# Kernel tuning notes

Measured on AMD Instinct MI355X. Metric: run time of the kernel, lower is better.

The kernel has to match this reference:

```python
import jax, jax.numpy as jnp
import numpy as np

HIDDEN = 1024
INTER = 4096
N_EXPERTS = 8
TOP_K = 2
INIT_STD = 0.02


def setup_inputs() -> dict:
    key = jax.random.key(0)
    ks = jax.random.split(key, 6)
    x = jax.random.normal(ks[0], (2, 1024, HIDDEN), dtype=jnp.float32)
    Wg = jax.random.normal(ks[1], (N_EXPERTS, HIDDEN), dtype=jnp.float32) * INIT_STD
    # Expert MLP params, stacked over experts. W1: [E, H, I], W2: [E, I, H].
    W1 = jax.random.normal(ks[2], (N_EXPERTS, HIDDEN, INTER), dtype=jnp.float32) * INIT_STD
    b1 = jnp.zeros((N_EXPERTS, INTER), dtype=jnp.float32)
    W2 = jax.random.normal(ks[3], (N_EXPERTS, INTER, HIDDEN), dtype=jnp.float32) * INIT_STD
    b2 = jnp.zeros((N_EXPERTS, HIDDEN), dtype=jnp.float32)
    return {"x": x, "Wg": Wg, "W1": W1, "b1": b1, "W2": W2, "b2": b2}


def reference(x, Wg, W1, b1, W2, b2):
    orig_shape = x.shape
    xt = x.reshape(-1, HIDDEN)              # [T, H]
    T = xt.shape[0]

    # Gating: top-k logits -> softmax over the k selected experts.
    logits = xt @ Wg.T                      # [T, E]
    topk_logits, topk_idx = jax.lax.top_k(logits, TOP_K)   # [T, K]
    w = jax.nn.softmax(topk_logits, axis=-1)               # [T, K]

    # Scatter top-k weights into a dense [T, E] gate matrix (zeros elsewhere).
    rows = jnp.arange(T)[:, None]
    gates = jnp.zeros((T, N_EXPERTS), xt.dtype).at[rows, topk_idx].add(w)

    # Dense expert compute (mathematically identical: non-selected experts get
    # gate weight 0). Expert MLP: Linear -> GELU (exact, erf) -> Linear.
    h = jnp.einsum('th,ehi->tei', xt, W1) + b1             # [T, E, I]
    h = jax.nn.gelu(h, approximate=False)
    o = jnp.einsum('tei,eih->teh', h, W2) + b2             # [T, E, H]
    y = jnp.einsum('te,teh->th', gates, o)                 # [T, H]
    return y.reshape(orig_shape)
```

## Files before the change

kernel.cpp:

```cpp
#include <hip/hip_runtime.h>
#include <hip/hip_bf16.h>

#define HID 1024
#define INTER 4096
#define NE 8
#define NTOK 2048
#define MAXROWS 5120

typedef __attribute__((ext_vector_type(8))) short short8v;
typedef __attribute__((ext_vector_type(4))) short short4v;
typedef __attribute__((ext_vector_type(4))) float f32x4;

__device__ __forceinline__ unsigned short f2bf(float f) {
  unsigned int u = __builtin_bit_cast(unsigned int, f);
  u = (u + 0x7FFFu + ((u >> 16) & 1u)) >> 16;
  return (unsigned short)u;
}
__device__ __forceinline__ float bf2f(unsigned short s) {
  unsigned int u = ((unsigned int)s) << 16;
  return __builtin_bit_cast(float, u);
}

typedef const __attribute__((address_space(1))) unsigned int* gas_t;
typedef __attribute__((address_space(3))) unsigned int* las_t;
__device__ __forceinline__ void gld16(const unsigned short* g, unsigned short* l) {
  __builtin_amdgcn_global_load_lds((gas_t)(const void*)g, (las_t)(void*)l, 16, 0, 0);
}

__device__ __forceinline__ void tconv_tile(const float* __restrict__ in,
                                           unsigned short* __restrict__ out,
                                           int R, int C, int bx, int by, int z,
                                           float* __restrict__ t) {
  const int r0 = by * 64, c0 = bx * 64;
  const int tr = threadIdx.x / 16;
  const int tc = (threadIdx.x % 16) * 4;
  const float* ip = in + ((size_t)z * R + r0) * (size_t)C + c0;
#pragma unroll
  for (int p = 0; p < 4; ++p) {
    f32x4 v = *(const f32x4*)&ip[(size_t)(p * 16 + tr) * C + tc];
    t[(p * 16 + tr) * 65 + tc + 0] = v[0];
    t[(p * 16 + tr) * 65 + tc + 1] = v[1];
    t[(p * 16 + tr) * 65 + tc + 2] = v[2];
    t[(p * 16 + tr) * 65 + tc + 3] = v[3];
  }
  __syncthreads();
  unsigned short* op = out + ((size_t)z * C + c0) * (size_t)R + r0;
#pragma unroll
  for (int p = 0; p < 4; ++p) {
    int c = p * 16 + tr;
    unsigned int a0 = (unsigned int)f2bf(t[(tc + 0) * 65 + c]) |
                      ((unsigned int)f2bf(t[(tc + 1) * 65 + c]) << 16);
    unsigned int a1 = (unsigned int)f2bf(t[(tc + 2) * 65 + c]) |
                      ((unsigned int)f2bf(t[(tc + 3) * 65 + c]) << 16);
    uint2 val; val.x = a0; val.y = a1;
    *(uint2*)&op[(size_t)c * R + tc] = val;
  }
}

__global__ __launch_bounds__(256) void prep_kernel(const float* __restrict__ x,
                                                   const float* __restrict__ W1,
                                                   const float* __restrict__ wg,
                                                   unsigned short* __restrict__ xb,
                                                   unsigned short* __restrict__ w1t,
                                                   int* __restrict__ tok_e,
                                                   float* __restrict__ tok_w) {
  __shared__ float sh[64 * 65];
  int bid = blockIdx.x;
  if (bid < 2048) {
    size_t i = (size_t)bid * 256 + threadIdx.x;
    f32x4 v = *(const f32x4*)&x[i * 4];
    uint2 r;
    r.x = (unsigned int)f2bf(v[0]) | ((unsigned int)f2bf(v[1]) << 16);
    r.y = (unsigned int)f2bf(v[2]) | ((unsigned int)f2bf(v[3]) << 16);
    *(uint2*)&xb[i * 4] = r;
    return;
  }
  bid -= 2048;
  if (bid < 8192) {
    tconv_tile(W1, w1t, HID, INTER, bid % 64, (bid / 64) % 16, bid / 1024, sh);
    return;
  }
  bid -= 8192;
  {
    const int t = bid;
    float acc[NE];
#pragma unroll
    for (int e = 0; e < NE; ++e) acc[e] = 0.f;
    for (int k = threadIdx.x; k < HID; k += 256) {
      float xv = x[(size_t)t * HID + k];
#pragma unroll
      for (int e = 0; e < NE; ++e) acc[e] += xv * wg[e * HID + k];
    }
#pragma unroll
    for (int e = 0; e < NE; ++e) {
#pragma unroll
      for (int off = 32; off >= 1; off >>= 1) acc[e] += __shfl_xor(acc[e], off, 64);
    }
    float* red = sh;
    const int wave = threadIdx.x >> 6, lane = threadIdx.x & 63;
    if (lane == 0) {
#pragma unroll
      for (int e = 0; e < NE; ++e) red[wave * NE + e] = acc[e];
    }
    __syncthreads();
    if (threadIdx.x == 0) {
      float l[NE];
#pragma unroll
      for (int e = 0; e < NE; ++e)
        l[e] = red[0 * NE + e] + red[1 * NE + e] + red[2 * NE + e] + red[3 * NE + e];
      int i0 = 0;
#pragma unroll
      for (int e = 1; e < NE; ++e) if (l[e] > l[i0]) i0 = e;
      int i1 = -1;
#pragma unroll
      for (int e = 0; e < NE; ++e) {
        if (e == i0) continue;
        if (i1 < 0 || l[e] > l[i1]) i1 = e;
      }
      float e1 = __expf(l[i1] - l[i0]);
      float w0 = 1.f / (1.f + e1);
      tok_e[t * 2 + 0] = i0;
      tok_e[t * 2 + 1] = i1;
      tok_w[t * 2 + 0] = w0;
      tok_w[t * 2 + 1] = 1.f - w0;
    }
  }
}

__global__ __launch_bounds__(512) void routing_kernel(const int* __restrict__ tok_e,
                                                      int* __restrict__ list_tok,
                                                      int* __restrict__ tok_gslot,
                                                      int* __restrict__ offs_out) {
  __shared__ int cnts[NE];
  __shared__ int offs_s[NE + 1];
  const int e = threadIdx.x >> 6, lane = threadIdx.x & 63;
  int c = 0;
  for (int base = 0; base < NTOK; base += 64) {
    int tok = base + lane;
    int e0 = tok_e[tok * 2], e1 = tok_e[tok * 2 + 1];
    bool m = (e0 == e) || (e1 == e);
    unsigned long long mask = __ballot(m);
    c += __popcll(mask);
  }
  if (lane == 0) cnts[e] = c;
  __syncthreads();
  if (threadIdx.x == 0) {
    int o = 0;
    for (int i = 0; i < NE; ++i) { offs_s[i] = o; o += (cnts[i] + 127) & ~127; }
    offs_s[NE] = o;
    for (int i = 0; i <= NE; ++i) offs_out[i] = offs_s[i];
  }
  __syncthreads();
  const int off = offs_s[e];
  int run = 0;
  for (int base = 0; base < NTOK; base += 64) {
    int tok = base + lane;
    int e0 = tok_e[tok * 2], e1 = tok_e[tok * 2 + 1];
    bool m = (e0 == e) || (e1 == e);
    unsigned long long mask = __ballot(m);
    int pos = run + __popcll(mask & ((1ull << lane) - 1ull));
    if (m) {
      int gs = off + pos;
      list_tok[gs] = tok;
      tok_gslot[tok * 2 + ((e0 == e) ? 0 : 1)] = gs;
    }
    run += __popcll(mask);
  }
  const int cnt = cnts[e];
  const int padded = (cnt + 127) & ~127;
  for (int p = cnt + lane; p < padded; p += 64) list_tok[off + p] = 0;
}

template <int KTOT, int NTOT, bool FIRST, int NSPLIT, int TCONVN>
__global__ __launch_bounds__(256, 3) void moe_gemm(const unsigned short* __restrict__ Abase,
                                                   const unsigned short* __restrict__ Bbase,
                                                   const float* __restrict__ bias,
                                                   const int* __restrict__ list_tok,
                                                   const int* __restrict__ offs,
                                                   void* __restrict__ outp,
                                                   const float* __restrict__ W2f,
                                                   unsigned short* __restrict__ w2t) {
  constexpr int KS = KTOT / NSPLIT;
  constexpr int NT = KS / 32;
  constexpr int nM = MAXROWS / 128;
  constexpr int nN = NTOT / 128;
  constexpr int NWG_GEMM = nN * nM * NSPLIT;
  __shared__ __align__(16) unsigned short lds[3][2][4096];

  if (TCONVN != 0 && blockIdx.x >= NWG_GEMM) {
    int t = blockIdx.x - NWG_GEMM;
    tconv_tile(W2f, w2t, INTER, HID, t % 16, (t / 16) % 64, t / 1024,
               (float*)&lds[0][0][0]);
    return;
  }

  int wg = blockIdx.x;
  wg = (wg & 7) * (NWG_GEMM >> 3) + (wg >> 3);
  const int ks = (NSPLIT > 1) ? (wg / (nM * nN)) : 0;
  const int rem = wg % (nM * nN);
  const int mt = rem % nM;
  const int nt = rem / nM;
  const int grow0 = mt * 128;
  if (grow0 >= offs[NE]) return;
  int e = 0;
#pragma unroll
  for (int i = 1; i < NE; ++i) if (grow0 >= offs[i]) e = i;
  const int n0 = nt * 128;
  const int k0 = ks * KS;

  const int tid = threadIdx.x;
  const int wave = tid >> 6, lane = tid & 63;

  const int srow = tid >> 2;
  const int skc = (((tid & 3) ^ ((srow >> 1) & 3)) * 8);
  const unsigned short* ag[2];
  const unsigned short* bg[2];
#pragma unroll
  for (int j = 0; j < 2; ++j) {
    const int row = srow + j * 64;
    size_t arow;
    if (FIRST) arow = (size_t)list_tok[grow0 + row] * KTOT;
    else       arow = (size_t)(grow0 + row) * KTOT;
    ag[j] = Abase + arow + k0 + skc;
    bg[j] = Bbase + (size_t)e * NTOT * KTOT + (size_t)(n0 + row) * KTOT + k0 + skc;
  }
  const int wbase = wave * 512;

  const int wm = wave >> 1, wn = wave & 1;
  const int fr = lane & 15;
  const int q = lane >> 4;
  int aoff[4], boff[4];
#pragma unroll
  for (int m = 0; m < 4; ++m) {
    const int row = wm * 64 + m * 16 + fr;
    aoff[m] = row * 32 + ((q ^ ((row >> 1) & 3)) * 8);
  }
#pragma unroll
  for (int n = 0; n < 4; ++n) {
    const int row = wn * 64 + n * 16 + fr;
    boff[n] = row * 32 + ((q ^ ((row >> 1) & 3)) * 8);
  }

  f32x4 acc[4][4] = {};

#define STAGE(S, SLOT)                                             \
  {                                                                \
    gld16(ag[0] + (S) * 32, &lds[SLOT][0][wbase]);                 \
    gld16(ag[1] + (S) * 32, &lds[SLOT][0][wbase + 2048]);          \
    gld16(bg[0] + (S) * 32, &lds[SLOT][1][wbase]);                 \
    gld16(bg[1] + (S) * 32, &lds[SLOT][1][wbase + 2048]);          \
  }

#define KITER(S, SL, DO_STAGE, VMSTR)                                 \
  {                                                                   \
    asm volatile("s_waitcnt vmcnt(" VMSTR ")" ::: "memory");          \
    asm volatile("s_barrier" ::: "memory");                           \
    const unsigned short* A = &lds[SL][0][0];                         \
    const unsigned short* B = &lds[SL][1][0];                         \
    short8v af[4], bf[4];                                             \
    _Pragma("unroll")                                                 \
    for (int m = 0; m < 4; ++m) af[m] = *(const short8v*)&A[aoff[m]]; \
    _Pragma("unroll")                                                 \
    for (int n = 0; n < 4; ++n) bf[n] = *(const short8v*)&B[boff[n]]; \
    if (DO_STAGE) {                                                   \
      int s2 = (SL) + 2; if (s2 >= 3) s2 -= 3;                        \
      STAGE((S) + 2, s2);                                             \
    }                                                                 \
    __builtin_amdgcn_s_setprio(1);                                    \
    _Pragma("unroll")                                                 \
    for (int n = 0; n < 4; ++n)                                       \
      _Pragma("unroll")                                               \
      for (int m = 0; m < 4; ++m)                                     \
        acc[m][n] = __builtin_amdgcn_mfma_f32_16x16x32_bf16(af[m], bf[n], acc[m][n], 0, 0, 0); \
    __builtin_amdgcn_s_setprio(0);                                    \
  }

  STAGE(0, 0);
  STAGE(1, 1);

  int sl = 0;
  for (int s = 0; s < NT - 2; ++s) {
    KITER(s, sl, true, "4");
    sl = sl + 1; if (sl >= 3) sl = 0;
  }
  KITER(NT - 2, sl, false, "4");
  sl = sl + 1; if (sl >= 3) sl = 0;
  KITER(NT - 1, sl, false, "0");

#undef KITER
#undef STAGE

  const int r4 = lane >> 4;
#pragma unroll
  for (int m = 0; m < 4; ++m) {
#pragma unroll
    for (int n = 0; n < 4; ++n) {
      const int gcol = n0 + wn * 64 + n * 16 + fr;
      float bv = 0.f;
      if (FIRST) bv = bias[e * NTOT + gcol];
#pragma unroll
      for (int r = 0; r < 4; ++r) {
        const int grow = grow0 + wm * 64 + m * 16 + r4 * 4 + r;
        float v = acc[m][n][r] + bv;
        if (FIRST) {
          v = 0.5f * v * (1.0f + erff(v * 0.70710678118654752f));
          ((unsigned short*)outp)[(size_t)grow * NTOT + gcol] = f2bf(v);
        } else {
          ((unsigned short*)outp)[((size_t)ks * MAXROWS + grow) * NTOT + gcol] = f2bf(v);
        }
      }
    }
  }
}

template <int NSPLIT>
__global__ __launch_bounds__(256) void combine_kernel(const unsigned short* __restrict__ part,
                                                      const int* __restrict__ tok_gslot,
                                                      const int* __restrict__ tok_e,
                                                      const float* __restrict__ tok_w,
                                                      const float* __restrict__ b2,
                                                      float* __restrict__ y) {
  const int t = blockIdx.x;
  const int c = threadIdx.x * 4;
  const int gs0 = tok_gslot[t * 2 + 0], gs1 = tok_gslot[t * 2 + 1];
  const int e0 = tok_e[t * 2 + 0], e1 = tok_e[t * 2 + 1];
  const float w0 = tok_w[t * 2 + 0], w1 = tok_w[t * 2 + 1];
  float s0[4] = {0.f, 0.f, 0.f, 0.f}, s1[4] = {0.f, 0.f, 0.f, 0.f};
#pragma unroll
  for (int ks = 0; ks < NSPLIT; ++ks) {
    short4v p0 = *(const short4v*)&part[((size_t)ks * MAXROWS + gs0) * HID + c];
    short4v p1 = *(const short4v*)&part[((size_t)ks * MAXROWS + gs1) * HID + c];
#pragma unroll
    for (int i = 0; i < 4; ++i) {
      s0[i] += bf2f((unsigned short)p0[i]);
      s1[i] += bf2f((unsigned short)p1[i]);
    }
  }
  f32x4 bb0 = *(const f32x4*)&b2[e0 * HID + c];
  f32x4 bb1 = *(const f32x4*)&b2[e1 * HID + c];
  f32x4 r;
#pragma unroll
  for (int i = 0; i < 4; ++i)
    r[i] = w0 * (s0[i] + bb0[i]) + w1 * (s1[i] + bb1[i]);
  *(f32x4*)&y[(size_t)t * HID + c] = r;
}

extern "C" void kernel_launch(void* const* d_in, const int* in_sizes, int n_in,
                              void* d_out, int out_size, void* d_ws, size_t ws_size,
                              hipStream_t stream) {
  const float* x  = (const float*)d_in[0];
  const float* wg = (const float*)d_in[1];
  const float* W1 = (const float*)d_in[2];
  const float* b1 = (const float*)d_in[3];
  const float* W2 = (const float*)d_in[4];
  const float* b2 = (const float*)d_in[5];
  float* y = (float*)d_out;

  unsigned char* ws = (unsigned char*)d_ws;
  size_t off = 0;
  unsigned short* w1t  = (unsigned short*)(ws + off);
  unsigned short* part = (unsigned short*)(ws + off); off += (size_t)NE * HID * INTER * 2;
  unsigned short* w2t  = (unsigned short*)(ws + off); off += (size_t)NE * INTER * HID * 2;
  unsigned short* xb   = (unsigned short*)(ws + off); off += (size_t)NTOK * HID * 2;
  unsigned short* h    = (unsigned short*)(ws + off); off += (size_t)MAXROWS * INTER * 2;
  int* tok_e           = (int*)(ws + off);            off += NTOK * 2 * 4;
  float* tok_w         = (float*)(ws + off);          off += NTOK * 2 * 4;
  int* tok_gslot       = (int*)(ws + off);            off += NTOK * 2 * 4;
  int* list_tok        = (int*)(ws + off);            off += MAXROWS * 4;
  int* offs            = (int*)(ws + off);            off += 64;
  (void)ws_size; (void)in_sizes; (void)n_in; (void)out_size;

  prep_kernel<<<2048 + 8192 + 2048, 256, 0, stream>>>(x, W1, wg, xb, w1t, tok_e, tok_w);
  routing_kernel<<<1, 512, 0, stream>>>(tok_e, list_tok, tok_gslot, offs);
  moe_gemm<HID, INTER, true, 1, 8192>
      <<<(INTER / 128) * (MAXROWS / 128) + 8192, 256, 0, stream>>>(
          xb, w1t, b1, list_tok, offs, (void*)h, W2, w2t);
  moe_gemm<INTER, HID, false, 4, 0>
      <<<(HID / 128) * (MAXROWS / 128) * 4, 256, 0, stream>>>(
          h, w2t, b2, list_tok, offs, (void*)part, nullptr, nullptr);
  combine_kernel<4><<<NTOK, 256, 0, stream>>>(part, tok_gslot, tok_e, tok_w, b2, y);
}
```

Baseline: 215.2 us.

## Double-buffer LDS fragment reads to overlap next-tile reads with current MFMAs

Restructures the GEMM K-loop so fragment registers are double-buffered. Each iteration reads the next k-slice's A/B fragments from LDS while the MFMAs consume the previous slice. The loop is unrolled by six to make the slot and buffer indices compile-time constants, and sched_barriers pin the instruction order. The global stage is issued before the wait. The aim is to hide LDS read latency behind matrix math, at the cost of more VGPRs, which may pressure occupancy at launch bounds 256,3.

```diff
diff --git a/kernel.cpp b/kernel.cpp
--- a/kernel.cpp
+++ b/kernel.cpp
@@ -182,6 +182,7 @@
                                                    unsigned short* __restrict__ w2t) {
   constexpr int KS = KTOT / NSPLIT;
   constexpr int NT = KS / 32;
+  static_assert(NT >= 8 && (NT - 2) % 6 == 0, "NT must be 6k+2");
   constexpr int nM = MAXROWS / 128;
   constexpr int nN = NTOT / 128;
   constexpr int NWG_GEMM = nN * nM * NSPLIT;
@@ -242,6 +243,7 @@
   }
 
   f32x4 acc[4][4] = {};
+  short8v af[2][4], bf[2][4];
 
 #define STAGE(S, SLOT)                                             \
   {                                                                \
@@ -251,43 +253,58 @@
     gld16(bg[1] + (S) * 32, &lds[SLOT][1][wbase + 2048]);          \
   }
 
-#define KITER(S, SL, DO_STAGE, VMSTR)                                 \
-  {                                                                   \
-    asm volatile("s_waitcnt vmcnt(" VMSTR ")" ::: "memory");          \
-    asm volatile("s_barrier" ::: "memory");                           \
-    const unsigned short* A = &lds[SL][0][0];                         \
-    const unsigned short* B = &lds[SL][1][0];                         \
-    short8v af[4], bf[4];                                             \
-    _Pragma("unroll")                                                 \
-    for (int m = 0; m < 4; ++m) af[m] = *(const short8v*)&A[aoff[m]]; \
-    _Pragma("unroll")                                                 \
-    for (int n = 0; n < 4; ++n) bf[n] = *(const short8v*)&B[boff[n]]; \
-    if (DO_STAGE) {                                                   \
-      int s2 = (SL) + 2; if (s2 >= 3) s2 -= 3;                        \
-      STAGE((S) + 2, s2);                                             \
-    }                                                                 \
-    __builtin_amdgcn_s_setprio(1);                                    \
-    _Pragma("unroll")                                                 \
-    for (int n = 0; n < 4; ++n)                                       \
-      _Pragma("unroll")                                               \
-      for (int m = 0; m < 4; ++m)                                     \
-        acc[m][n] = __builtin_amdgcn_mfma_f32_16x16x32_bf16(af[m], bf[n], acc[m][n], 0, 0, 0); \
-    __builtin_amdgcn_s_setprio(0);                                    \
+#define READF(BK, SLN)                                                          \
+  {                                                                             \
+    _Pragma("unroll")                                                           \
+    for (int m = 0; m < 4; ++m) af[BK][m] = *(const short8v*)&lds[SLN][0][aoff[m]]; \
+    _Pragma("unroll")                                                           \
+    for (int n = 0; n < 4; ++n) bf[BK][n] = *(const short8v*)&lds[SLN][1][boff[n]]; \
+  }
+
+#define MFMAC(BK)                                                  \
+  {                                                                \
+    __builtin_amdgcn_s_setprio(1);                                 \
+    _Pragma("unroll")                                              \
+    for (int n = 0; n < 4; ++n)                                    \
+      _Pragma("unroll")                                            \
+      for (int m = 0; m < 4; ++m)                                  \
+        acc[m][n] = __builtin_amdgcn_mfma_f32_16x16x32_bf16(af[BK][m], bf[BK][n], acc[m][n], 0, 0, 0); \
+    __builtin_amdgcn_s_setprio(0);                                 \
+  }
+
+#define ITER(S, SL, CUR, DOSTAGE, VMSTR)                           \
+  {                                                                \
+    if (DOSTAGE) STAGE((S) + 2, (((SL) + 2) % 3));                 \
+    asm volatile("s_waitcnt vmcnt(" VMSTR ")" ::: "memory");       \
+    asm volatile("s_barrier" ::: "memory");                        \
+    __builtin_amdgcn_sched_barrier(0);                             \
+    READF(1 - (CUR), (((SL) + 1) % 3));                            \
+    __builtin_amdgcn_sched_barrier(0);                             \
+    MFMAC(CUR);                                                    \
   }
 
   STAGE(0, 0);
   STAGE(1, 1);
-
-  int sl = 0;
-  for (int s = 0; s < NT - 2; ++s) {
-    KITER(s, sl, true, "4");
-    sl = sl + 1; if (sl >= 3) sl = 0;
-  }
-  KITER(NT - 2, sl, false, "4");
-  sl = sl + 1; if (sl >= 3) sl = 0;
-  KITER(NT - 1, sl, false, "0");
-
-#undef KITER
+  asm volatile("s_waitcnt vmcnt(4)" ::: "memory");
+  asm volatile("s_barrier" ::: "memory");
+  __builtin_amdgcn_sched_barrier(0);
+  READF(0, 0);
+  __builtin_amdgcn_sched_barrier(0);
+
+  for (int s = 0; s < NT - 2; s += 6) {
+    ITER(s + 0, 0, 0, true, "4");
+    ITER(s + 1, 1, 1, true, "4");
+    ITER(s + 2, 2, 0, true, "4");
+    ITER(s + 3, 0, 1, true, "4");
+    ITER(s + 4, 1, 0, true, "4");
+    ITER(s + 5, 2, 1, true, "4");
+  }
+  ITER(NT - 2, 0, 0, false, "0");
+  MFMAC(1);
+
+#undef ITER
+#undef MFMAC
+#undef READF
 #undef STAGE
 
   const int r4 = lane >> 4;
```

Result: no change. 216.7 us (+0.7%).

## Give each wave private LDS tiles and drop workgroup barriers in MoE GEMM

Applied to the files above, without the earlier changes.

Restructures the GEMM main loop so each wave stages its own 64-row slices of A and B into a private double-buffered LDS region. This replaces the shared triple-buffered tiles and removes the per-iteration s_barrier; waves sync only through their own vmcnt/lgkmcnt waits. The cost is redundant loads: tiles that waves previously shared are now fetched twice from global/L2. LDS per workgroup also grows, so launch bounds drop from 3 to 2 workgroups per CU, and prefetch depth falls from two stages to one.

```diff
diff --git a/kernel.cpp b/kernel.cpp
--- a/kernel.cpp
+++ b/kernel.cpp
@@ -172,7 +172,7 @@
 }
 
 template <int KTOT, int NTOT, bool FIRST, int NSPLIT, int TCONVN>
-__global__ __launch_bounds__(256, 3) void moe_gemm(const unsigned short* __restrict__ Abase,
+__global__ __launch_bounds__(256, 2) void moe_gemm(const unsigned short* __restrict__ Abase,
                                                    const unsigned short* __restrict__ Bbase,
                                                    const float* __restrict__ bias,
                                                    const int* __restrict__ list_tok,
@@ -182,15 +182,16 @@
                                                    unsigned short* __restrict__ w2t) {
   constexpr int KS = KTOT / NSPLIT;
   constexpr int NT = KS / 32;
+  static_assert(NT >= 4 && (NT & 1) == 0, "NT must be even");
   constexpr int nM = MAXROWS / 128;
   constexpr int nN = NTOT / 128;
   constexpr int NWG_GEMM = nN * nM * NSPLIT;
-  __shared__ __align__(16) unsigned short lds[3][2][4096];
+  __shared__ __align__(16) unsigned short lds[4][2][2][2048];
 
   if (TCONVN != 0 && blockIdx.x >= NWG_GEMM) {
     int t = blockIdx.x - NWG_GEMM;
     tconv_tile(W2f, w2t, INTER, HID, t % 16, (t / 16) % 64, t / 1024,
-               (float*)&lds[0][0][0]);
+               (float*)&lds[0][0][0][0]);
     return;
   }
 
@@ -210,62 +211,52 @@
 
   const int tid = threadIdx.x;
   const int wave = tid >> 6, lane = tid & 63;
-
-  const int srow = tid >> 2;
-  const int skc = (((tid & 3) ^ ((srow >> 1) & 3)) * 8);
-  const unsigned short* ag[2];
-  const unsigned short* bg[2];
-#pragma unroll
-  for (int j = 0; j < 2; ++j) {
-    const int row = srow + j * 64;
+  const int wm = wave >> 1, wn = wave & 1;
+
+  const int rl = lane >> 2;
+  const int sc = (((lane & 3) ^ ((lane >> 3) & 3)) * 8);
+  const unsigned short* ag[4];
+  const unsigned short* bg[4];
+#pragma unroll
+  for (int i = 0; i < 4; ++i) {
+    const int arl = wm * 64 + i * 16 + rl;
     size_t arow;
-    if (FIRST) arow = (size_t)list_tok[grow0 + row] * KTOT;
-    else       arow = (size_t)(grow0 + row) * KTOT;
-    ag[j] = Abase + arow + k0 + skc;
-    bg[j] = Bbase + (size_t)e * NTOT * KTOT + (size_t)(n0 + row) * KTOT + k0 + skc;
-  }
-  const int wbase = wave * 512;
-
-  const int wm = wave >> 1, wn = wave & 1;
+    if (FIRST) arow = (size_t)list_tok[grow0 + arl] * KTOT;
+    else       arow = (size_t)(grow0 + arl) * KTOT;
+    ag[i] = Abase + arow + k0 + sc;
+    const int brl = wn * 64 + i * 16 + rl;
+    bg[i] = Bbase + (size_t)e * NTOT * KTOT + (size_t)(n0 + brl) * KTOT + k0 + sc;
+  }
+
   const int fr = lane & 15;
   const int q = lane >> 4;
-  int aoff[4], boff[4];
+  int foff[4];
 #pragma unroll
   for (int m = 0; m < 4; ++m) {
-    const int row = wm * 64 + m * 16 + fr;
-    aoff[m] = row * 32 + ((q ^ ((row >> 1) & 3)) * 8);
-  }
-#pragma unroll
-  for (int n = 0; n < 4; ++n) {
-    const int row = wn * 64 + n * 16 + fr;
-    boff[n] = row * 32 + ((q ^ ((row >> 1) & 3)) * 8);
+    const int row = m * 16 + fr;
+    foff[m] = row * 32 + ((q ^ ((row >> 1) & 3)) * 8);
   }
 
   f32x4 acc[4][4] = {};
 
-#define STAGE(S, SLOT)                                             \
+#define STAGE(S, SL)                                               \
   {                                                                \
-    gld16(ag[0] + (S) * 32, &lds[SLOT][0][wbase]);                 \
-    gld16(ag[1] + (S) * 32, &lds[SLOT][0][wbase + 2048]);          \
-    gld16(bg[0] + (S) * 32, &lds[SLOT][1][wbase]);                 \
-    gld16(bg[1] + (S) * 32, &lds[SLOT][1][wbase + 2048]);          \
-  }
-
-#define KITER(S, SL, DO_STAGE, VMSTR)                                 \
+    _Pragma("unroll")                                              \
+    for (int i = 0; i < 4; ++i) {                                  \
+      gld16(ag[i] + (S) * 32, &lds[wave][SL][0][i * 512]);         \
+      gld16(bg[i] + (S) * 32, &lds[wave][SL][1][i * 512]);         \
+    }                                                              \
+  }
+
+#define COMPUTE(SL)                                                   \
   {                                                                   \
-    asm volatile("s_waitcnt vmcnt(" VMSTR ")" ::: "memory");          \
-    asm volatile("s_barrier" ::: "memory");                           \
-    const unsigned short* A = &lds[SL][0][0];                         \
-    const unsigned short* B = &lds[SL][1][0];                         \
+    const unsigned short* A = &lds[wave][SL][0][0];                   \
+    const unsigned short* B = &lds[wave][SL][1][0];                   \
     short8v af[4], bf[4];                                             \
     _Pragma("unroll")                                                 \
-    for (int m = 0; m < 4; ++m) af[m] = *(const short8v*)&A[aoff[m]]; \
+    for (int m = 0; m < 4; ++m) af[m] = *(const short8v*)&A[foff[m]]; \
     _Pragma("unroll")                                                 \
-    for (int n = 0; n < 4; ++n) bf[n] = *(const short8v*)&B[boff[n]]; \
-    if (DO_STAGE) {                                                   \
-      int s2 = (SL) + 2; if (s2 >= 3) s2 -= 3;                        \
-      STAGE((S) + 2, s2);                                             \
-    }                                                                 \
+    for (int n = 0; n < 4; ++n) bf[n] = *(const short8v*)&B[foff[n]]; \
     __builtin_amdgcn_s_setprio(1);                                    \
     _Pragma("unroll")                                                 \
     for (int n = 0; n < 4; ++n)                                       \
@@ -275,19 +266,25 @@
     __builtin_amdgcn_s_setprio(0);                                    \
   }
 
+#define VMW(NSTR)                                                  \
+  asm volatile("s_waitcnt vmcnt(" NSTR ")" ::: "memory");          \
+  __builtin_amdgcn_sched_barrier(0);
+#define LKW                                                        \
+  asm volatile("s_waitcnt lgkmcnt(0)" ::: "memory");               \
+  __builtin_amdgcn_sched_barrier(0);
+
   STAGE(0, 0);
-  STAGE(1, 1);
-
-  int sl = 0;
-  for (int s = 0; s < NT - 2; ++s) {
-    KITER(s, sl, true, "4");
-    sl = sl + 1; if (sl >= 3) sl = 0;
-  }
-  KITER(NT - 2, sl, false, "4");
-  sl = sl + 1; if (sl >= 3) sl = 0;
-  KITER(NT - 1, sl, false, "0");
-
-#undef KITER
+  for (int s = 0; s < NT; s += 2) {
+    if (s + 1 < NT) { STAGE(s + 1, 1); VMW("8") } else { VMW("0") }
+    COMPUTE(0);
+    if (s + 2 < NT) { LKW; STAGE(s + 2, 0); VMW("8") } else { VMW("0") }
+    COMPUTE(1);
+    LKW;
+  }
+
+#undef VMW
+#undef LKW
+#undef COMPUTE
 #undef STAGE
 
   const int r4 = lane >> 4;
```

Measured after the change: 258.9 us. +20.3%, slower.

## Move MoE GEMMs to 256x256 tiles with 512-thread blocks and double buffering

Applied to the files above, without the earlier changes.

The grouped expert GEMM moves from 128x128 tiles with 256 threads and a 3-slot, 32-deep K pipeline to 256x256 tiles with 512 threads (8 waves, each computing 128x64), using a 2-slot, 64-deep K buffer split into half-phases. Expert row padding grows to 256 and MAXROWS to 6144. The second GEMM's split-K goes from 4 to 8, and the W2 transpose that rides inside the first GEMM launch is rewritten as a per-wave 64x32 transpose. The aim is more operand reuse per LDS byte and fewer global loads per FLOP. In exchange it spends more on padding rows, adds more split-K partials for the combine step to read, and may lower occupancy.

```diff
diff --git a/kernel.cpp b/kernel.cpp
--- a/kernel.cpp
+++ b/kernel.cpp
@@ -5,7 +5,7 @@
 #define INTER 4096
 #define NE 8
 #define NTOK 2048
-#define MAXROWS 5120
+#define MAXROWS 6144
 
 typedef __attribute__((ext_vector_type(8))) short short8v;
 typedef __attribute__((ext_vector_type(4))) short short4v;
@@ -54,6 +54,42 @@
                       ((unsigned int)f2bf(t[(tc + 3) * 65 + c]) << 16);
     uint2 val; val.x = a0; val.y = a1;
     *(uint2*)&op[(size_t)c * R + tc] = val;
+  }
+}
+
+__device__ __forceinline__ void wave_tconv2(const float* __restrict__ in,
+                                            unsigned short* __restrict__ out,
+                                            int gidx, float* __restrict__ sc, int lane) {
+  const int e = gidx >> 11;
+  const int r = gidx & 2047;
+  const int i0 = (r >> 5) * 64, h0 = (r & 31) * 32;
+  const float* ip = in + ((size_t)e * INTER + i0) * HID + h0;
+  f32x4 v[8];
+#pragma unroll
+  for (int p = 0; p < 8; ++p)
+    v[p] = *(const f32x4*)&ip[(size_t)(p * 8 + (lane >> 3)) * HID + (lane & 7) * 4];
+#pragma unroll
+  for (int p = 0; p < 8; ++p) {
+    const int row = p * 8 + (lane >> 3), col = (lane & 7) * 4;
+#pragma unroll
+    for (int j = 0; j < 4; ++j) sc[row * 37 + col + j] = v[p][j];
+  }
+  asm volatile("s_waitcnt lgkmcnt(0)" ::: "memory");
+  __builtin_amdgcn_sched_barrier(0);
+  unsigned short* op = out + ((size_t)e * HID + h0) * INTER + i0;
+#pragma unroll
+  for (int p = 0; p < 4; ++p) {
+    const int c = p * 8 + (lane >> 3);
+    const int r8 = (lane & 7) * 8;
+    uint4 w;
+    unsigned int* wp = (unsigned int*)&w;
+#pragma unroll
+    for (int j = 0; j < 4; ++j) {
+      unsigned int lo = f2bf(sc[(r8 + 2 * j) * 37 + c]);
+      unsigned int hi = f2bf(sc[(r8 + 2 * j + 1) * 37 + c]);
+      wp[j] = lo | (hi << 16);
+    }
+    *(uint4*)&op[(size_t)c * INTER + r8] = w;
   }
 }
 
@@ -146,7 +182,7 @@
   __syncthreads();
   if (threadIdx.x == 0) {
     int o = 0;
-    for (int i = 0; i < NE; ++i) { offs_s[i] = o; o += (cnts[i] + 127) & ~127; }
+    for (int i = 0; i < NE; ++i) { offs_s[i] = o; o += (cnts[i] + 255) & ~255; }
     offs_s[NE] = o;
     for (int i = 0; i <= NE; ++i) offs_out[i] = offs_s[i];
   }
@@ -167,12 +203,12 @@
     run += __popcll(mask);
   }
   const int cnt = cnts[e];
-  const int padded = (cnt + 127) & ~127;
+  const int padded = (cnt + 255) & ~255;
   for (int p = cnt + lane; p < padded; p += 64) list_tok[off + p] = 0;
 }
 
-template <int KTOT, int NTOT, bool FIRST, int NSPLIT, int TCONVN>
-__global__ __launch_bounds__(256, 3) void moe_gemm(const unsigned short* __restrict__ Abase,
+template <int KTOT, int NTOT, bool FIRST, int NSPLIT, bool TCONV>
+__global__ __launch_bounds__(512, 2) void moe_gemm(const unsigned short* __restrict__ Abase,
                                                    const unsigned short* __restrict__ Bbase,
                                                    const float* __restrict__ bias,
                                                    const int* __restrict__ list_tok,
@@ -181,118 +217,115 @@
                                                    const float* __restrict__ W2f,
                                                    unsigned short* __restrict__ w2t) {
   constexpr int KS = KTOT / NSPLIT;
-  constexpr int NT = KS / 32;
-  constexpr int nM = MAXROWS / 128;
-  constexpr int nN = NTOT / 128;
-  constexpr int NWG_GEMM = nN * nM * NSPLIT;
-  __shared__ __align__(16) unsigned short lds[3][2][4096];
-
-  if (TCONVN != 0 && blockIdx.x >= NWG_GEMM) {
-    int t = blockIdx.x - NWG_GEMM;
-    tconv_tile(W2f, w2t, INTER, HID, t % 16, (t / 16) % 64, t / 1024,
-               (float*)&lds[0][0][0]);
+  constexpr int T = KS / 64;
+  constexpr int nM = MAXROWS / 256;
+  constexpr int nN = NTOT / 256;
+  constexpr int NWG = nM * nN * NSPLIT;
+  __shared__ __align__(16) unsigned short lds[65536];
+
+  const int tid = threadIdx.x;
+  const int wid = tid >> 6, lane = tid & 63;
+
+  if (TCONV && (int)blockIdx.x >= NWG) {
+    wave_tconv2(W2f, w2t, ((int)blockIdx.x - NWG) * 8 + wid,
+                (float*)lds + wid * (64 * 37), lane);
     return;
   }
 
   int wg = blockIdx.x;
-  wg = (wg & 7) * (NWG_GEMM >> 3) + (wg >> 3);
-  const int ks = (NSPLIT > 1) ? (wg / (nM * nN)) : 0;
+  wg = (wg & 7) * (NWG >> 3) + (wg >> 3);
+  const int ksid = (NSPLIT > 1) ? (wg / (nM * nN)) : 0;
   const int rem = wg % (nM * nN);
   const int mt = rem % nM;
   const int nt = rem / nM;
-  const int grow0 = mt * 128;
+  const int grow0 = mt * 256;
   if (grow0 >= offs[NE]) return;
   int e = 0;
 #pragma unroll
   for (int i = 1; i < NE; ++i) if (grow0 >= offs[i]) e = i;
-  const int n0 = nt * 128;
-  const int k0 = ks * KS;
-
-  const int tid = threadIdx.x;
-  const int wave = tid >> 6, lane = tid & 63;
-
-  const int srow = tid >> 2;
-  const int skc = (((tid & 3) ^ ((srow >> 1) & 3)) * 8);
+  const int n0 = nt * 256;
+  const int k0 = ksid * KS;
+
+  const int jsrc = (((tid & 3) ^ ((tid >> 3) & 3)) * 8);
   const unsigned short* ag[2];
   const unsigned short* bg[2];
 #pragma unroll
-  for (int j = 0; j < 2; ++j) {
-    const int row = srow + j * 64;
+  for (int c = 0; c < 2; ++c) {
+    const int R = c * 128 + (tid >> 2);
     size_t arow;
-    if (FIRST) arow = (size_t)list_tok[grow0 + row] * KTOT;
-    else       arow = (size_t)(grow0 + row) * KTOT;
-    ag[j] = Abase + arow + k0 + skc;
-    bg[j] = Bbase + (size_t)e * NTOT * KTOT + (size_t)(n0 + row) * KTOT + k0 + skc;
-  }
-  const int wbase = wave * 512;
-
-  const int wm = wave >> 1, wn = wave & 1;
-  const int fr = lane & 15;
-  const int q = lane >> 4;
+    if (FIRST) arow = (size_t)list_tok[grow0 + R] * KTOT;
+    else       arow = (size_t)(grow0 + R) * KTOT;
+    ag[c] = Abase + arow + k0 + jsrc;
+    bg[c] = Bbase + (size_t)e * NTOT * KTOT + (size_t)(n0 + R) * KTOT + k0 + jsrc;
+  }
+
+  const int fr = lane & 15, q4 = lane >> 4;
+  const int csw = (q4 ^ ((fr >> 1) & 3)) * 8;
+  const int wm = wid >> 2, wn = wid & 3;
   int aoff[4], boff[4];
 #pragma unroll
-  for (int m = 0; m < 4; ++m) {
-    const int row = wm * 64 + m * 16 + fr;
-    aoff[m] = row * 32 + ((q ^ ((row >> 1) & 3)) * 8);
-  }
-#pragma unroll
-  for (int n = 0; n < 4; ++n) {
-    const int row = wn * 64 + n * 16 + fr;
-    boff[n] = row * 32 + ((q ^ ((row >> 1) & 3)) * 8);
-  }
-
-  f32x4 acc[4][4] = {};
-
-#define STAGE(S, SLOT)                                             \
-  {                                                                \
-    gld16(ag[0] + (S) * 32, &lds[SLOT][0][wbase]);                 \
-    gld16(ag[1] + (S) * 32, &lds[SLOT][0][wbase + 2048]);          \
-    gld16(bg[0] + (S) * 32, &lds[SLOT][1][wbase]);                 \
-    gld16(bg[1] + (S) * 32, &lds[SLOT][1][wbase + 2048]);          \
-  }
-
-#define KITER(S, SL, DO_STAGE, VMSTR)                                 \
-  {                                                                   \
-    asm volatile("s_waitcnt vmcnt(" VMSTR ")" ::: "memory");          \
-    asm volatile("s_barrier" ::: "memory");                           \
-    const unsigned short* A = &lds[SL][0][0];                         \
-    const unsigned short* B = &lds[SL][1][0];                         \
-    short8v af[4], bf[4];                                             \
-    _Pragma("unroll")                                                 \
-    for (int m = 0; m < 4; ++m) af[m] = *(const short8v*)&A[aoff[m]]; \
-    _Pragma("unroll")                                                 \
-    for (int n = 0; n < 4; ++n) bf[n] = *(const short8v*)&B[boff[n]]; \
-    if (DO_STAGE) {                                                   \
-      int s2 = (SL) + 2; if (s2 >= 3) s2 -= 3;                        \
-      STAGE((S) + 2, s2);                                             \
-    }                                                                 \
-    __builtin_amdgcn_s_setprio(1);                                    \
-    _Pragma("unroll")                                                 \
-    for (int n = 0; n < 4; ++n)                                       \
-      _Pragma("unroll")                                               \
-      for (int m = 0; m < 4; ++m)                                     \
-        acc[m][n] = __builtin_amdgcn_mfma_f32_16x16x32_bf16(af[m], bf[n], acc[m][n], 0, 0, 0); \
-    __builtin_amdgcn_s_setprio(0);                                    \
-  }
-
-  STAGE(0, 0);
-  STAGE(1, 1);
-
-  int sl = 0;
-  for (int s = 0; s < NT - 2; ++s) {
-    KITER(s, sl, true, "4");
-    sl = sl + 1; if (sl >= 3) sl = 0;
-  }
-  KITER(NT - 2, sl, false, "4");
-  sl = sl + 1; if (sl >= 3) sl = 0;
-  KITER(NT - 1, sl, false, "0");
-
-#undef KITER
-#undef STAGE
-
-  const int r4 = lane >> 4;
-#pragma unroll
-  for (int m = 0; m < 4; ++m) {
+  for (int m = 0; m < 4; ++m) aoff[m] = (wm * 128 + m * 16 + fr) * 32 + csw;
+#pragma unroll
+  for (int n = 0; n < 4; ++n) boff[n] = 16384 + (wn * 64 + n * 16 + fr) * 32 + csw;
+
+  f32x4 acc[8][4] = {};
+
+#define STG(MAT, KH, D1, TOFF)                                                          \
+  {                                                                                     \
+    const unsigned short* s0 = ((MAT) ? bg[0] : ag[0]) + (TOFF) + (KH) * 32;            \
+    const unsigned short* s1 = ((MAT) ? bg[1] : ag[1]) + (TOFF) + (KH) * 32;            \
+    unsigned short* db = lds + (D1) * 32768 + (MAT) * 16384 + (KH) * 8192 + wid * 512;  \
+    gld16(s0, db);                                                                      \
+    gld16(s1, db + 4096);                                                               \
+  }
+
+#define PH(DD, KSS, MH, DOSTG, SMAT, SKH, TOFF)                                         \
+  {                                                                                     \
+    const unsigned short* Lp = lds + (DD) * 32768 + (KSS) * 8192;                       \
+    short8v af[4], bf[4];                                                               \
+    _Pragma("unroll")                                                                   \
+    for (int m = 0; m < 4; ++m) af[m] = *(const short8v*)&Lp[(MH) * 2048 + aoff[m]];    \
+    _Pragma("unroll")                                                                   \
+    for (int n = 0; n < 4; ++n) bf[n] = *(const short8v*)&Lp[boff[n]];                  \
+    if (DOSTG) STG(SMAT, SKH, (DD) ^ 1, TOFF);                                          \
+    asm volatile("s_waitcnt lgkmcnt(0)" ::: "memory");                                  \
+    __builtin_amdgcn_sched_barrier(0);                                                  \
+    __builtin_amdgcn_s_setprio(1);                                                      \
+    _Pragma("unroll")                                                                   \
+    for (int n = 0; n < 4; ++n)                                                         \
+      _Pragma("unroll")                                                                 \
+      for (int m = 0; m < 4; ++m)                                                       \
+        acc[(MH) * 4 + m][n] = __builtin_amdgcn_mfma_f32_16x16x32_bf16(                 \
+            af[m], bf[n], acc[(MH) * 4 + m][n], 0, 0, 0);                               \
+    __builtin_amdgcn_s_setprio(0);                                                      \
+  }
+
+  STG(0, 0, 0, 0); STG(1, 0, 0, 0); STG(0, 1, 0, 0); STG(1, 1, 0, 0);
+  asm volatile("s_waitcnt vmcnt(4)" ::: "memory");
+  asm volatile("s_barrier" ::: "memory");
+
+  for (int t = 0; t < T; ++t) {
+    const int d = t & 1;
+    const int toff = (t + 1) * 64;
+    const bool hn = (t + 1 < T);
+    PH(d, 0, 0, hn, 0, 0, toff);
+    PH(d, 0, 1, hn, 1, 0, toff);
+    if (hn) asm volatile("s_waitcnt vmcnt(4)" ::: "memory");
+    else    asm volatile("s_waitcnt vmcnt(0)" ::: "memory");
+    asm volatile("s_barrier" ::: "memory");
+    PH(d, 1, 0, hn, 0, 1, toff);
+    PH(d, 1, 1, hn, 1, 1, toff);
+    if (hn) {
+      asm volatile("s_waitcnt vmcnt(4)" ::: "memory");
+      asm volatile("s_barrier" ::: "memory");
+    }
+  }
+
+#undef PH
+#undef STG
+
+#pragma unroll
+  for (int m = 0; m < 8; ++m) {
 #pragma unroll
     for (int n = 0; n < 4; ++n) {
       const int gcol = n0 + wn * 64 + n * 16 + fr;
@@ -300,13 +333,13 @@
       if (FIRST) bv = bias[e * NTOT + gcol];
 #pragma unroll
       for (int r = 0; r < 4; ++r) {
-        const int grow = grow0 + wm * 64 + m * 16 + r4 * 4 + r;
+        const int grow = grow0 + wm * 128 + m * 16 + q4 * 4 + r;
         float v = acc[m][n][r] + bv;
         if (FIRST) {
           v = 0.5f * v * (1.0f + erff(v * 0.70710678118654752f));
           ((unsigned short*)outp)[(size_t)grow * NTOT + gcol] = f2bf(v);
         } else {
-          ((unsigned short*)outp)[((size_t)ks * MAXROWS + grow) * NTOT + gcol] = f2bf(v);
+          ((unsigned short*)outp)[((size_t)ksid * MAXROWS + grow) * NTOT + gcol] = f2bf(v);
         }
       }
     }
@@ -359,8 +392,9 @@
   unsigned char* ws = (unsigned char*)d_ws;
   size_t off = 0;
   unsigned short* w1t  = (unsigned short*)(ws + off);
-  unsigned short* part = (unsigned short*)(ws + off); off += (size_t)NE * HID * INTER * 2;
-  unsigned short* w2t  = (unsigned short*)(ws + off); off += (size_t)NE * INTER * HID * 2;
+  unsigned short* part = (unsigned short*)(ws + off);
+  off += (size_t)8 * MAXROWS * HID * 2;
+  unsigned short* w2t  = (unsigned short*)(ws + off); off += (size_t)NE * HID * INTER * 2;
   unsigned short* xb   = (unsigned short*)(ws + off); off += (size_t)NTOK * HID * 2;
   unsigned short* h    = (unsigned short*)(ws + off); off += (size_t)MAXROWS * INTER * 2;
   int* tok_e           = (int*)(ws + off);            off += NTOK * 2 * 4;
@@ -372,11 +406,11 @@
 
   prep_kernel<<<2048 + 8192 + 2048, 256, 0, stream>>>(x, W1, wg, xb, w1t, tok_e, tok_w);
   routing_kernel<<<1, 512, 0, stream>>>(tok_e, list_tok, tok_gslot, offs);
-  moe_gemm<HID, INTER, true, 1, 8192>
-      <<<(INTER / 128) * (MAXROWS / 128) + 8192, 256, 0, stream>>>(
+  moe_gemm<HID, INTER, true, 1, true>
+      <<<(MAXROWS / 256) * (INTER / 256) + 2048, 512, 0, stream>>>(
           xb, w1t, b1, list_tok, offs, (void*)h, W2, w2t);
-  moe_gemm<INTER, HID, false, 4, 0>
-      <<<(HID / 128) * (MAXROWS / 128) * 4, 256, 0, stream>>>(
+  moe_gemm<INTER, HID, false, 8, false>
+      <<<(MAXROWS / 256) * (HID / 256) * 8, 512, 0, stream>>>(
           h, w2t, b2, list_tok, offs, (void*)part, nullptr, nullptr);
-  combine_kernel<4><<<NTOK, 256, 0, stream>>>(part, tok_gslot, tok_e, tok_w, b2, y);
-}
+  combine_kernel<8><<<NTOK, 256, 0, stream>>>(part, tok_gslot, tok_e, tok_w, b2, y);
+}
```

After: 237.3 us. 1.1x slower.
